# Performance work log

Measured on AMD Instinct MI355X. Metric: run time of the kernel, lower is better.

Reference implementation:

```python
import jax, jax.numpy as jnp
import numpy as np

NODES_PER_GRAPH = 116
HEADS = 2
D_HEAD = 116  # out_channels per head
HID = 256
B = 512
N = B * NODES_PER_GRAPH
DEG = 8
E = N * DEG
D_OUT = HEADS * D_HEAD  # 232


def setup_inputs() -> dict:
    key = jax.random.key(0)
    ks = jax.random.split(key, 6)
    h_flat = jax.random.normal(ks[0], (N, HID), dtype=jnp.float32)
    # every node receives DEG edges from random nodes within its own 116-node graph
    dst = jnp.repeat(jnp.arange(N, dtype=jnp.int64), DEG)
    offs = jax.random.randint(ks[1], (E,), 0, NODES_PER_GRAPH, dtype=jnp.int64)
    src = (dst // NODES_PER_GRAPH) * NODES_PER_GRAPH + offs
    edge_index = jnp.stack([src, dst], axis=0)
    batch_index = jnp.repeat(jnp.arange(B, dtype=jnp.int64), NODES_PER_GRAPH)
    s = 1.0 / np.sqrt(HID)
    Wq = jax.random.normal(ks[2], (HID, D_OUT), dtype=jnp.float32) * s
    Wk = jax.random.normal(ks[3], (HID, D_OUT), dtype=jnp.float32) * s
    Wv = jax.random.normal(ks[4], (HID, D_OUT), dtype=jnp.float32) * s
    Ws = jax.random.normal(ks[5], (HID, D_OUT), dtype=jnp.float32) * s
    return {"h_flat": h_flat, "edge_index": edge_index, "batch_index": batch_index,
            "Wq": Wq, "Wk": Wk, "Wv": Wv, "Ws": Ws}


def _graph_transformer_layer(h, edge_index, Wq, Wk, Wv, Ws):
    # PyG TransformerConv-style multi-head edge attention, concat heads + root skip.
    n = h.shape[0]
    q = (h @ Wq).reshape(n, HEADS, D_HEAD)
    k = (h @ Wk).reshape(n, HEADS, D_HEAD)
    v = (h @ Wv).reshape(n, HEADS, D_HEAD)
    src, dst = edge_index[0], edge_index[1]
    # per-edge scores [E, H]
    scores = jnp.einsum('ehd,ehd->eh', q[dst], k[src]) / np.sqrt(D_HEAD)
    # segment softmax over incoming edges of each dst node
    m = jax.ops.segment_max(scores, dst, num_segments=n)
    m = jnp.where(jnp.isfinite(m), m, 0.0)
    ex = jnp.exp(scores - m[dst])
    denom = jax.ops.segment_sum(ex, dst, num_segments=n)
    alpha_e = ex / (denom[dst] + 1e-16)
    msg = alpha_e[:, :, None] * v[src]                      # [E, H, Dh]
    attn = jax.ops.segment_sum(msg, dst, num_segments=n)    # [N, H, Dh]
    return attn.reshape(n, D_OUT) + h @ Ws


def reference(h_flat, edge_index, batch_index, Wq, Wk, Wv, Ws):
    n = h_flat.shape[0]
    b = n // NODES_PER_GRAPH
    h_proj = _graph_transformer_layer(h_flat, edge_index, Wq, Wk, Wv, Ws)  # [N, 232]
    e = h_proj.mean(axis=-1)                                 # [N]
    # scatter_softmax over per-graph node segments
    em = jax.ops.segment_max(e, batch_index, num_segments=b)
    ee = jnp.exp(e - em[batch_index])
    es = jax.ops.segment_sum(ee, batch_index, num_segments=b)
    alpha = ee / es[batch_index]                             # [N]
    h_weighted = alpha[:, None] * h_proj                     # [N, 232]
    alpha_map = alpha.reshape(b, NODES_PER_GRAPH)            # [B, 116]
    return alpha_map, h_weighted
```

## Files before the change

### kernel.cpp

```cpp
#include <hip/hip_runtime.h>

#define NODES  116
#define HEADS  2
#define DH     116
#define HID    256
#define NGRAPH 512
#define NN     (NGRAPH*NODES)
#define DEG    8
#define DOUT   (HEADS*DH)
#define RSTR   136

typedef short  s8v  __attribute__((ext_vector_type(8)));
typedef float  f4v  __attribute__((ext_vector_type(4)));

static __device__ __forceinline__ float bf2f(unsigned short u) {
    union { unsigned int i; float f; } c; c.i = ((unsigned int)u) << 16; return c.f;
}
static __device__ __forceinline__ unsigned short f2bf(float f) {
    union { float f; unsigned int u; } c; c.f = f;
    unsigned int u = c.u;
    unsigned int r = (u + 0x7FFFu + ((u >> 16) & 1u)) >> 16;
    return (unsigned short)r;
}

#define GLD_LDS16(gptr, lptr) \
    __builtin_amdgcn_global_load_lds((const __attribute__((address_space(1))) void*)(gptr), \
                                     (__attribute__((address_space(3))) void*)(lptr), 16, 0, 0)

__global__ __launch_bounds__(256) void prep_w(const float* __restrict__ Wq,
                                              const float* __restrict__ Wk,
                                              const float* __restrict__ Wv,
                                              const float* __restrict__ Ws,
                                              unsigned short* __restrict__ wt)
{
    unsigned int f = blockIdx.x * 256 + threadIdx.x;
    unsigned int n    = f & 127;
    unsigned int quad = (f >> 7) & 3;
    unsigned int kb   = (f >> 9) & 7;
    unsigned int ch   = (f >> 12) & 3;
    unsigned int hd   = f >> 14;
    unsigned short o[8] = {0,0,0,0,0,0,0,0};
    if (n < NODES) {
        unsigned int col = hd * DH + n;
        unsigned int k   = kb * 32 + quad * 8;
        const float* W = (ch == 0) ? Wq : (ch == 1) ? Wk : (ch == 2) ? Wv : Ws;
        #pragma unroll
        for (int i = 0; i < 8; i++)
            o[i] = f2bf(W[(size_t)(k + i) * DOUT + col]);
    }
    *(uint4*)(wt + (size_t)f * 8) = *(const uint4*)o;
}

__global__ __launch_bounds__(1024, 8) void k1_gemm(
    const float* __restrict__ h,
    const unsigned short* __restrict__ wt,
    unsigned short* __restrict__ qkvs)
{
    __shared__ __align__(16) unsigned short stA[8*4*116*8 + 96];
    __shared__ __align__(16) unsigned short stB[2*4096];

    const int b   = blockIdx.x;
    const int g   = b >> 1;
    const int hd  = b & 1;
    const int tid = threadIdx.x;
    const int w    = tid >> 6;
    const int lane = tid & 63;
    const int l15  = lane & 15;
    const int quad = lane >> 4;
    const int wm   = w >> 2;
    const int wn   = w & 3;

    {
        const int am = tid >> 3;
        const int q8 = tid & 7;
        if (am < NODES) {
            const float* hrow = h + ((size_t)g * NODES + am) * HID + q8 * 4;
            #pragma unroll
            for (int kb = 0; kb < 8; kb++) {
                float4 av = *(const float4*)(hrow + kb * 32);
                unsigned short o[4] = { f2bf(av.x), f2bf(av.y), f2bf(av.z), f2bf(av.w) };
                *(uint2*)(stA + kb * (4*116*8) + ((q8 >> 1) * 116 + am) * 8 + (q8 & 1) * 4) =
                    *(const uint2*)o;
            }
        }
    }

    const size_t wbase = (size_t)hd * 4 * 8 * 4096;

    if (w < 8) {
        const unsigned short* src = wt + wbase + w * 512;
        GLD_LDS16((const char*)src + lane * 16, (char*)stB + w * 1024);
    }
    __syncthreads();

    f4v acc[2][2];
    #pragma unroll
    for (int i = 0; i < 2; i++)
        #pragma unroll
        for (int j = 0; j < 2; j++)
            #pragma unroll
            for (int r = 0; r < 4; r++) acc[i][j][r] = 0.f;

    for (int t = 0; t < 32; t++) {
        const int kb = t & 7;
        const unsigned short* cur = stB + (t & 1) * 4096;
        if (t < 31 && w < 8) {
            const unsigned short* src = wt + wbase + (size_t)(t + 1) * 4096 + w * 512;
            GLD_LDS16((const char*)src + lane * 16,
                      (char*)stB + ((t & 1) ^ 1) * 8192 + w * 1024);
        }
        const unsigned short* sa = stA + kb * (4*116*8);
        s8v a0 = *(const s8v*)(sa + (quad * 116 + wm * 32 + l15) * 8);
        s8v a1 = *(const s8v*)(sa + (quad * 116 + wm * 32 + 16 + l15) * 8);
        s8v b0 = *(const s8v*)(cur + (quad * 128 + wn * 32 + l15) * 8);
        s8v b1 = *(const s8v*)(cur + (quad * 128 + wn * 32 + 16 + l15) * 8);
        acc[0][0] = __builtin_amdgcn_mfma_f32_16x16x32_bf16(a0, b0, acc[0][0], 0, 0, 0);
        acc[0][1] = __builtin_amdgcn_mfma_f32_16x16x32_bf16(a0, b1, acc[0][1], 0, 0, 0);
        acc[1][0] = __builtin_amdgcn_mfma_f32_16x16x32_bf16(a1, b0, acc[1][0], 0, 0, 0);
        acc[1][1] = __builtin_amdgcn_mfma_f32_16x16x32_bf16(a1, b1, acc[1][1], 0, 0, 0);
        if (kb == 7) {
            const int ch = t >> 3;
            #pragma unroll
            for (int i = 0; i < 2; i++) {
                #pragma unroll
                for (int j = 0; j < 2; j++) {
                    int col = wn * 32 + j * 16 + l15;
                    #pragma unroll
                    for (int r = 0; r < 4; r++) {
                        int row = wm * 32 + i * 16 + quad * 4 + r;
                        if (row < NODES && col < NODES)
                            qkvs[(((size_t)g * NODES + row) * 2 + hd) * 464 + ch * 116 + col] =
                                f2bf(acc[i][j][r]);
                        acc[i][j][r] = 0.f;
                    }
                }
            }
        }
        __syncthreads();
    }
}

__global__ __launch_bounds__(1024, 8) void k2_attn(
    const unsigned short* __restrict__ qkvs,
    const int* __restrict__ eidx,
    unsigned short* __restrict__ hpj,
    float* __restrict__ psums)
{
    __shared__ __align__(16) unsigned short ql[128*RSTR];
    __shared__ __align__(16) unsigned short kl[128*RSTR];
    __shared__ int   srcl[NODES*DEG];
    __shared__ float scf[NODES*DEG];

    const int b   = blockIdx.x;
    const int g   = b >> 1;
    const int hd  = b & 1;
    const int tid = threadIdx.x;
    const int w    = tid >> 6;
    const int lane = tid & 63;
    const int l15  = lane & 15;
    const int quad = lane >> 4;
    const int wm   = w >> 2;
    const int wn   = w & 3;

    if (tid < NODES * DEG)
        srcl[tid] = eidx[(size_t)g * NODES * DEG + tid] - g * NODES;

    const size_t nb = ((size_t)g * NODES) * 2 + hd;

    for (int f = tid; f < NODES * 29; f += 1024) {
        int r = f / 29, c = f - r * 29;
        *(uint2*)(ql + r * RSTR + c * 4) =
            *(const uint2*)(qkvs + (nb + (size_t)r * 2) * 464 + 0 * 116 + c * 4);
        *(uint2*)(kl + r * RSTR + c * 4) =
            *(const uint2*)(qkvs + (nb + (size_t)r * 2) * 464 + 1 * 116 + c * 4);
    }
    for (int f = tid; f < 128 * 3; f += 1024) {
        int r = f / 3, j = f - r * 3;
        *(uint2*)(ql + r * RSTR + 116 + j * 4) = make_uint2(0u, 0u);
        *(uint2*)(kl + r * RSTR + 116 + j * 4) = make_uint2(0u, 0u);
    }
    __syncthreads();

    f4v sacc[2][2];
    #pragma unroll
    for (int i = 0; i < 2; i++)
        #pragma unroll
        for (int j = 0; j < 2; j++)
            #pragma unroll
            for (int r = 0; r < 4; r++) sacc[i][j][r] = 0.f;
    #pragma unroll
    for (int ks = 0; ks < 4; ks++) {
        s8v a0 = *(const s8v*)(ql + (wm * 32 + l15) * RSTR + ks * 32 + quad * 8);
        s8v a1 = *(const s8v*)(ql + (wm * 32 + 16 + l15) * RSTR + ks * 32 + quad * 8);
        s8v b0 = *(const s8v*)(kl + (wn * 32 + l15) * RSTR + ks * 32 + quad * 8);
        s8v b1 = *(const s8v*)(kl + (wn * 32 + 16 + l15) * RSTR + ks * 32 + quad * 8);
        sacc[0][0] = __builtin_amdgcn_mfma_f32_16x16x32_bf16(a0, b0, sacc[0][0], 0, 0, 0);
        sacc[0][1] = __builtin_amdgcn_mfma_f32_16x16x32_bf16(a0, b1, sacc[0][1], 0, 0, 0);
        sacc[1][0] = __builtin_amdgcn_mfma_f32_16x16x32_bf16(a1, b0, sacc[1][0], 0, 0, 0);
        sacc[1][1] = __builtin_amdgcn_mfma_f32_16x16x32_bf16(a1, b1, sacc[1][1], 0, 0, 0);
    }
    #pragma unroll
    for (int i = 0; i < 2; i++) {
        #pragma unroll
        for (int r = 0; r < 4; r++) {
            int row = wm * 32 + i * 16 + quad * 4 + r;
            if (row < NODES) {
                #pragma unroll
                for (int j = 0; j < 2; j++) {
                    int col = wn * 32 + j * 16 + l15;
                    #pragma unroll
                    for (int e = 0; e < DEG; e++)
                        if (srcl[row * DEG + e] == col)
                            scf[row * DEG + e] = sacc[i][j][r];
                }
            }
        }
    }
    __syncthreads();

    for (int f = tid; f < 128 * RSTR / 8; f += 1024)
        *(uint4*)(kl + (size_t)f * 8) = make_uint4(0u, 0u, 0u, 0u);
    for (int f = tid; f < NODES * 29; f += 1024) {
        int r = f / 29, c = f - r * 29;
        uint2 vv = *(const uint2*)(qkvs + (nb + (size_t)r * 2) * 464 + 2 * 116 + c * 4);
        const unsigned short* vp = (const unsigned short*)&vv;
        #pragma unroll
        for (int i = 0; i < 4; i++)
            ql[(c * 4 + i) * RSTR + r] = vp[i];
    }
    if (tid < 12 * 17) {
        int r = 116 + tid / 17, c = tid - (tid / 17) * 17;
        *(uint4*)(ql + r * RSTR + c * 8) = make_uint4(0u, 0u, 0u, 0u);
    }
    __syncthreads();

    if (tid < NODES * DEG) {
        float s = scf[tid] * 0.09284766908852594f;
        float m = s;
        m = fmaxf(m, __shfl_xor(m, 1));
        m = fmaxf(m, __shfl_xor(m, 2));
        m = fmaxf(m, __shfl_xor(m, 4));
        float e = __expf(s - m);
        float sum = e;
        sum += __shfl_xor(sum, 1);
        sum += __shfl_xor(sum, 2);
        sum += __shfl_xor(sum, 4);
        scf[tid] = e / sum;
    }
    __syncthreads();

    if (tid < NODES) {
        #pragma unroll
        for (int j = 0; j < DEG; j++) {
            int sj = srcl[tid * DEG + j];
            bool first = true;
            for (int jj = 0; jj < j; jj++) first = first && (srcl[tid * DEG + jj] != sj);
            if (first) {
                float a = scf[tid * DEG + j];
                for (int jj = j + 1; jj < DEG; jj++)
                    if (srcl[tid * DEG + jj] == sj) a += scf[tid * DEG + jj];
                kl[tid * RSTR + sj] = f2bf(a);
            }
        }
    }
    __syncthreads();

    f4v accs[2][2];
    #pragma unroll
    for (int i = 0; i < 2; i++)
        #pragma unroll
        for (int j = 0; j < 2; j++)
            #pragma unroll
            for (int r = 0; r < 4; r++) accs[i][j][r] = 0.f;
    #pragma unroll
    for (int ks = 0; ks < 4; ks++) {
        s8v a0 = *(const s8v*)(kl + (wm * 32 + l15) * RSTR + ks * 32 + quad * 8);
        s8v a1 = *(const s8v*)(kl + (wm * 32 + 16 + l15) * RSTR + ks * 32 + quad * 8);
        s8v b0 = *(const s8v*)(ql + (wn * 32 + l15) * RSTR + ks * 32 + quad * 8);
        s8v b1 = *(const s8v*)(ql + (wn * 32 + 16 + l15) * RSTR + ks * 32 + quad * 8);
        accs[0][0] = __builtin_amdgcn_mfma_f32_16x16x32_bf16(a0, b0, accs[0][0], 0, 0, 0);
        accs[0][1] = __builtin_amdgcn_mfma_f32_16x16x32_bf16(a0, b1, accs[0][1], 0, 0, 0);
        accs[1][0] = __builtin_amdgcn_mfma_f32_16x16x32_bf16(a1, b0, accs[1][0], 0, 0, 0);
        accs[1][1] = __builtin_amdgcn_mfma_f32_16x16x32_bf16(a1, b1, accs[1][1], 0, 0, 0);
    }
    __syncthreads();

    for (int f = tid; f < NODES * 29; f += 1024) {
        int r = f / 29, c = f - r * 29;
        *(uint2*)(kl + r * RSTR + c * 4) =
            *(const uint2*)(qkvs + (nb + (size_t)r * 2) * 464 + 3 * 116 + c * 4);
    }
    __syncthreads();

    #pragma unroll
    for (int i = 0; i < 2; i++) {
        #pragma unroll
        for (int j = 0; j < 2; j++) {
            int col = wn * 32 + j * 16 + l15;
            #pragma unroll
            for (int r = 0; r < 4; r++) {
                int row = wm * 32 + i * 16 + quad * 4 + r;
                float v = accs[i][j][r];
                if (row < NODES && col < NODES) v += bf2f(kl[row * RSTR + col]);
                ql[row * RSTR + col] = f2bf(v);
            }
        }
    }
    __syncthreads();

    if (tid < NODES * DEG) {
        const int i   = tid >> 3;
        const int seg = tid & 7;
        float rs = 0.0f;
        #pragma unroll
        for (int t = 0; t < 2; t++) {
            int gi = seg + t * 8;
            if (gi < 15) {
                const s8v v8 = *(const s8v*)(ql + i * RSTR + gi * 8);
                #pragma unroll
                for (int e = 0; e < 8; e++) rs += bf2f((unsigned short)v8[e]);
            }
        }
        rs += __shfl_xor(rs, 1);
        rs += __shfl_xor(rs, 2);
        rs += __shfl_xor(rs, 4);
        if (seg == 0) psums[((size_t)hd * NGRAPH + g) * NODES + i] = rs;
    }
    for (int f = tid; f < NODES * 29; f += 1024) {
        int r  = f / 29;
        int gi = f - r * 29;
        *(uint2*)(hpj + ((size_t)(g * NODES + r)) * DOUT + hd * DH + gi * 4) =
            *(const uint2*)(ql + r * RSTR + gi * 4);
    }
}

__global__ __launch_bounds__(256) void pool_k3(const unsigned short* __restrict__ hp,
                                               const float* __restrict__ psums,
                                               float* __restrict__ out_alpha,
                                               float* __restrict__ out_hw)
{
    __shared__ float ew[NODES];
    __shared__ float alph[NODES];
    __shared__ float red[2];

    const int g   = blockIdx.x;
    const int tid = threadIdx.x;

    if (tid < NODES)
        ew[tid] = (psums[(size_t)g * NODES + tid] +
                   psums[((size_t)NGRAPH + g) * NODES + tid]) * (1.0f / DOUT);
    __syncthreads();
    if (tid < 64) {
        float a = ew[tid];
        float b = (tid + 64 < NODES) ? ew[tid + 64] : -1e30f;
        float mm = fmaxf(a, b);
        #pragma unroll
        for (int off = 32; off > 0; off >>= 1) mm = fmaxf(mm, __shfl_down(mm, off));
        if (tid == 0) red[0] = mm;
    }
    __syncthreads();
    if (tid < NODES) ew[tid] = __expf(ew[tid] - red[0]);
    __syncthreads();
    if (tid < 64) {
        float a = ew[tid] + ((tid + 64 < NODES) ? ew[tid + 64] : 0.0f);
        #pragma unroll
        for (int off = 32; off > 0; off >>= 1) a += __shfl_down(a, off);
        if (tid == 0) red[1] = a;
    }
    __syncthreads();
    if (tid < NODES) {
        float al = ew[tid] / red[1];
        alph[tid] = al;
        out_alpha[(size_t)g * NODES + tid] = al;
    }
    __syncthreads();

    for (int f = tid; f < NODES * 58; f += 256) {
        int r  = f / 58;
        int gi = f - r * 58;
        float al = alph[r];
        uint2 hv = *(const uint2*)(hp + ((size_t)(g * NODES + r)) * DOUT + gi * 4);
        float4 o = make_float4(al * bf2f((unsigned short)(hv.x & 0xFFFF)),
                               al * bf2f((unsigned short)(hv.x >> 16)),
                               al * bf2f((unsigned short)(hv.y & 0xFFFF)),
                               al * bf2f((unsigned short)(hv.y >> 16)));
        *(float4*)(out_hw + ((size_t)(g * NODES + r)) * DOUT + gi * 4) = o;
    }
}

__global__ __launch_bounds__(1024, 4) void fused_all(
    const float* __restrict__ h,
    const unsigned short* __restrict__ wt,
    const int* __restrict__ eidx,
    unsigned short* __restrict__ hp,
    float* __restrict__ out_alpha,
    float* __restrict__ out_hw)
{
    __shared__ __align__(16) unsigned short stA[8*4096];
    __shared__ __align__(16) unsigned short ovl[2*128*RSTR];
    __shared__ int   srcl[NODES*DEG];
    __shared__ float scf[NODES*DEG];
    __shared__ float ps[2][NODES];
    __shared__ float red[2];

    unsigned short* const ql = ovl;
    unsigned short* const kl = ovl + 128 * RSTR;

    const int g   = blockIdx.x;
    const int tid = threadIdx.x;
    const int w    = tid >> 6;
    const int lane = tid & 63;
    const int l15  = lane & 15;
    const int quad = lane >> 4;
    const int wm   = w >> 2;
    const int wn   = w & 3;

    if (tid < NODES * DEG)
        srcl[tid] = eidx[(size_t)g * NODES * DEG + tid] - g * NODES;

    {
        const int am = tid >> 3;
        const int q8 = tid & 7;
        long grow = (long)g * NODES + am;
        if (grow >= NN) grow = NN - 1;
        const float* hrow = h + (size_t)grow * HID + q8 * 4;
        const int aoff = ((q8 >> 1) * 128 + am) * 8 + (q8 & 1) * 4;
        float4 a8[8];
        #pragma unroll
        for (int kb = 0; kb < 8; kb++) a8[kb] = *(const float4*)(hrow + kb * 32);
        #pragma unroll
        for (int kb = 0; kb < 8; kb++) {
            unsigned short o[4] = { f2bf(a8[kb].x), f2bf(a8[kb].y),
                                    f2bf(a8[kb].z), f2bf(a8[kb].w) };
            *(uint2*)(stA + kb * 4096 + aoff) = *(const uint2*)o;
        }
    }

    #pragma unroll
    for (int hd = 0; hd < 2; hd++) {
        const size_t wbase = (size_t)hd * 4 * 8 * 4096;

        f4v accq[2][2], acck[2][2], accv[2][2], accs[2][2];
        #pragma unroll
        for (int i = 0; i < 2; i++)
            #pragma unroll
            for (int j = 0; j < 2; j++)
                #pragma unroll
                for (int r = 0; r < 4; r++) {
                    accq[i][j][r] = 0.f; acck[i][j][r] = 0.f;
                    accv[i][j][r] = 0.f; accs[i][j][r] = 0.f;
                }

        #pragma unroll
        for (int j = 0; j < 2; j++) {
            int c = w * 2 + j;
            int ch = c >> 3, sub = c & 7;
            const unsigned short* src = wt + wbase + ((size_t)(ch * 8)) * 4096 + sub * 512;
            GLD_LDS16((const char*)src + lane * 16, (char*)ovl + c * 1024);
        }
        __syncthreads();

        #pragma unroll
        for (int kb = 0; kb < 8; kb++) {
            const unsigned short* curb = ovl + (kb & 1) * 16384;
            unsigned short* nxtb = ovl + ((kb & 1) ^ 1) * 16384;
            if (kb < 7) {
                #pragma unroll
                for (int j = 0; j < 2; j++) {
                    int c = w * 2 + j;
                    int ch = c >> 3, sub = c & 7;
                    const unsigned short* src = wt + wbase + ((size_t)(ch * 8 + kb + 1)) * 4096 + sub * 512;
                    GLD_LDS16((const char*)src + lane * 16, (char*)nxtb + c * 1024);
                }
            }
            const unsigned short* sa = stA + kb * 4096;
            s8v a0 = *(const s8v*)(sa + (quad * 128 + wm * 32 + l15) * 8);
            s8v a1 = *(const s8v*)(sa + (quad * 128 + wm * 32 + 16 + l15) * 8);
            #define CHUNK_MFMA(ACC, CH) { \
                s8v b0 = *(const s8v*)(curb + (CH) * 4096 + (quad * 128 + wn * 32 + l15) * 8); \
                s8v b1 = *(const s8v*)(curb + (CH) * 4096 + (quad * 128 + wn * 32 + 16 + l15) * 8); \
                ACC[0][0] = __builtin_amdgcn_mfma_f32_16x16x32_bf16(a0, b0, ACC[0][0], 0, 0, 0); \
                ACC[0][1] = __builtin_amdgcn_mfma_f32_16x16x32_bf16(a0, b1, ACC[0][1], 0, 0, 0); \
                ACC[1][0] = __builtin_amdgcn_mfma_f32_16x16x32_bf16(a1, b0, ACC[1][0], 0, 0, 0); \
                ACC[1][1] = __builtin_amdgcn_mfma_f32_16x16x32_bf16(a1, b1, ACC[1][1], 0, 0, 0); }
            CHUNK_MFMA(accq, 0)
            CHUNK_MFMA(acck, 1)
            CHUNK_MFMA(accv, 2)
            CHUNK_MFMA(accs, 3)
            #undef CHUNK_MFMA
            __syncthreads();
        }

        #pragma unroll
        for (int i = 0; i < 2; i++) {
            #pragma unroll
            for (int j = 0; j < 2; j++) {
                int col = wn * 32 + j * 16 + l15;
                #pragma unroll
                for (int r = 0; r < 4; r++) {
                    int row = wm * 32 + i * 16 + quad * 4 + r;
                    ql[row * RSTR + col] = (col < NODES) ? f2bf(accq[i][j][r]) : 0;
                    kl[row * RSTR + col] = (col < NODES) ? f2bf(acck[i][j][r]) : 0;
                }
            }
        }
        __syncthreads();

        f4v sacc[2][2];
        #pragma unroll
        for (int i = 0; i < 2; i++)
            #pragma unroll
            for (int j = 0; j < 2; j++)
                #pragma unroll
                for (int r = 0; r < 4; r++) sacc[i][j][r] = 0.f;
        #pragma unroll
        for (int ks = 0; ks < 4; ks++) {
            s8v a0 = *(const s8v*)(ql + (wm * 32 + l15) * RSTR + ks * 32 + quad * 8);
            s8v a1 = *(const s8v*)(ql + (wm * 32 + 16 + l15) * RSTR + ks * 32 + quad * 8);
            s8v b0 = *(const s8v*)(kl + (wn * 32 + l15) * RSTR + ks * 32 + quad * 8);
            s8v b1 = *(const s8v*)(kl + (wn * 32 + 16 + l15) * RSTR + ks * 32 + quad * 8);
            sacc[0][0] = __builtin_amdgcn_mfma_f32_16x16x32_bf16(a0, b0, sacc[0][0], 0, 0, 0);
            sacc[0][1] = __builtin_amdgcn_mfma_f32_16x16x32_bf16(a0, b1, sacc[0][1], 0, 0, 0);
            sacc[1][0] = __builtin_amdgcn_mfma_f32_16x16x32_bf16(a1, b0, sacc[1][0], 0, 0, 0);
            sacc[1][1] = __builtin_amdgcn_mfma_f32_16x16x32_bf16(a1, b1, sacc[1][1], 0, 0, 0);
        }
        #pragma unroll
        for (int i = 0; i < 2; i++) {
            #pragma unroll
            for (int r = 0; r < 4; r++) {
                int row = wm * 32 + i * 16 + quad * 4 + r;
                if (row < NODES) {
                    #pragma unroll
                    for (int j = 0; j < 2; j++) {
                        int col = wn * 32 + j * 16 + l15;
                        #pragma unroll
                        for (int e = 0; e < DEG; e++)
                            if (srcl[row * DEG + e] == col)
                                scf[row * DEG + e] = sacc[i][j][r];
                    }
                }
            }
        }
        __syncthreads();

        for (int f = tid; f < 128 * RSTR / 8; f += 1024)
            *(uint4*)(kl + (size_t)f * 8) = make_uint4(0u, 0u, 0u, 0u);
        #pragma unroll
        for (int i = 0; i < 2; i++) {
            #pragma unroll
            for (int j = 0; j < 2; j++) {
                int col = wn * 32 + j * 16 + l15;
                #pragma unroll
                for (int r = 0; r < 4; r++) {
                    int row = wm * 32 + i * 16 + quad * 4 + r;
                    ql[col * RSTR + row] = (row < NODES) ? f2bf(accv[i][j][r]) : 0;
                }
            }
        }
        __syncthreads();

        if (tid < NODES * DEG) {
            float s = scf[tid] * 0.09284766908852594f;
            float m = s;
            m = fmaxf(m, __shfl_xor(m, 1));
            m = fmaxf(m, __shfl_xor(m, 2));
            m = fmaxf(m, __shfl_xor(m, 4));
            float e = __expf(s - m);
            float sum = e;
            sum += __shfl_xor(sum, 1);
            sum += __shfl_xor(sum, 2);
            sum += __shfl_xor(sum, 4);
            scf[tid] = e / sum;
        }
        __syncthreads();

        if (tid < NODES) {
            #pragma unroll
            for (int j = 0; j < DEG; j++) {
                int sj = srcl[tid * DEG + j];
                bool first = true;
                for (int jj = 0; jj < j; jj++) first = first && (srcl[tid * DEG + jj] != sj);
                if (first) {
                    float a = scf[tid * DEG + j];
                    for (int jj = j + 1; jj < DEG; jj++)
                        if (srcl[tid * DEG + jj] == sj) a += scf[tid * DEG + jj];
                    kl[tid * RSTR + sj] = f2bf(a);
                }
            }
        }
        __syncthreads();

        #pragma unroll
        for (int ks = 0; ks < 4; ks++) {
            s8v a0 = *(const s8v*)(kl + (wm * 32 + l15) * RSTR + ks * 32 + quad * 8);
            s8v a1 = *(const s8v*)(kl + (wm * 32 + 16 + l15) * RSTR + ks * 32 + quad * 8);
            s8v b0 = *(const s8v*)(ql + (wn * 32 + l15) * RSTR + ks * 32 + quad * 8);
            s8v b1 = *(const s8v*)(ql + (wn * 32 + 16 + l15) * RSTR + ks * 32 + quad * 8);
            accs[0][0] = __builtin_amdgcn_mfma_f32_16x16x32_bf16(a0, b0, accs[0][0], 0, 0, 0);
            accs[0][1] = __builtin_amdgcn_mfma_f32_16x16x32_bf16(a0, b1, accs[0][1], 0, 0, 0);
            accs[1][0] = __builtin_amdgcn_mfma_f32_16x16x32_bf16(a1, b0, accs[1][0], 0, 0, 0);
            accs[1][1] = __builtin_amdgcn_mfma_f32_16x16x32_bf16(a1, b1, accs[1][1], 0, 0, 0);
        }
        __syncthreads();

        #pragma unroll
        for (int i = 0; i < 2; i++) {
            #pragma unroll
            for (int j = 0; j < 2; j++) {
                int col = wn * 32 + j * 16 + l15;
                #pragma unroll
                for (int r = 0; r < 4; r++) {
                    int row = wm * 32 + i * 16 + quad * 4 + r;
                    ql[row * RSTR + col] = f2bf(accs[i][j][r]);
                }
            }
        }
        __syncthreads();

        if (tid < NODES * DEG) {
            const int i   = tid >> 3;
            const int seg = tid & 7;
            float rs = 0.0f;
            #pragma unroll
            for (int t = 0; t < 2; t++) {
                int gi = seg + t * 8;
                if (gi < 15) {
                    const s8v v8 = *(const s8v*)(ql + i * RSTR + gi * 8);
                    #pragma unroll
                    for (int e = 0; e < 8; e++) rs += bf2f((unsigned short)v8[e]);
                }
            }
            rs += __shfl_xor(rs, 1);
            rs += __shfl_xor(rs, 2);
            rs += __shfl_xor(rs, 4);
            if (seg == 0) ps[hd][i] = rs;
        }
        if (hd == 0) {
            for (int f = tid; f < NODES * 29; f += 1024) {
                int r  = f / 29;
                int gi = f - r * 29;
                *(uint2*)(hp + ((size_t)g * NODES + r) * 116 + gi * 4) =
                    *(const uint2*)(ql + r * RSTR + gi * 4);
            }
        }
        __syncthreads();
    }

    if (tid < NODES) scf[tid] = (ps[0][tid] + ps[1][tid]) * (1.0f / DOUT);
    __syncthreads();
    if (tid < 64) {
        float a = scf[tid];
        float b = (tid + 64 < NODES) ? scf[tid + 64] : -1e30f;
        float mm = fmaxf(a, b);
        #pragma unroll
        for (int off = 32; off > 0; off >>= 1) mm = fmaxf(mm, __shfl_down(mm, off));
        if (tid == 0) red[0] = mm;
    }
    __syncthreads();
    if (tid < NODES) scf[tid] = __expf(scf[tid] - red[0]);
    __syncthreads();
    if (tid < 64) {
        float a = scf[tid] + ((tid + 64 < NODES) ? scf[tid + 64] : 0.0f);
        #pragma unroll
        for (int off = 32; off > 0; off >>= 1) a += __shfl_down(a, off);
        if (tid == 0) red[1] = a;
    }
    __syncthreads();
    if (tid < NODES) {
        float al = scf[tid] / red[1];
        scf[tid] = al;
        out_alpha[(size_t)g * NODES + tid] = al;
    }
    __syncthreads();
    for (int f = tid; f < NODES * 58; f += 1024) {
        int r  = f / 58;
        int gi = f - r * 58;
        float al = scf[r];
        float4 o;
        if (gi < 29) {
            uint2 hv = *(const uint2*)(hp + ((size_t)g * NODES + r) * 116 + gi * 4);
            o = make_float4(al * bf2f((unsigned short)(hv.x & 0xFFFF)),
                            al * bf2f((unsigned short)(hv.x >> 16)),
                            al * bf2f((unsigned short)(hv.y & 0xFFFF)),
                            al * bf2f((unsigned short)(hv.y >> 16)));
        } else {
            const unsigned short* hv = ql + r * RSTR + (gi - 29) * 4;
            o = make_float4(al * bf2f(hv[0]), al * bf2f(hv[1]),
                            al * bf2f(hv[2]), al * bf2f(hv[3]));
        }
        *(float4*)(out_hw + ((size_t)g * NODES + r) * DOUT + gi * 4) = o;
    }
}

extern "C" void kernel_launch(void* const* d_in, const int* in_sizes, int n_in,
                              void* d_out, int out_size, void* d_ws, size_t ws_size,
                              hipStream_t stream)
{
    const float* h    = (const float*)d_in[0];
    const int*   eidx = (const int*)d_in[1];
    const float* Wq   = (const float*)d_in[3];
    const float* Wk   = (const float*)d_in[4];
    const float* Wv   = (const float*)d_in[5];
    const float* Ws   = (const float*)d_in[6];

    float* out_alpha = (float*)d_out;
    float* out_hw    = out_alpha + NN;

    const size_t WT_ELS   = 262144;
    const size_t QKVS_ELS = (size_t)NN * 2 * 464;
    const size_t HPJ_ELS  = (size_t)NN * DOUT;
    const size_t NEED = (WT_ELS + QKVS_ELS + HPJ_ELS) * 2 + (size_t)2 * NGRAPH * NODES * 4;

    unsigned short* wt = (unsigned short*)d_ws;
    prep_w<<<128, 256, 0, stream>>>(Wq, Wk, Wv, Ws, wt);

    if (ws_size >= NEED) {
        unsigned short* qkvs = wt + WT_ELS;
        unsigned short* hpj  = qkvs + QKVS_ELS;
        float*          ps   = (float*)(hpj + HPJ_ELS);
        k1_gemm<<<2*NGRAPH, 1024, 0, stream>>>(h, wt, qkvs);
        k2_attn<<<2*NGRAPH, 1024, 0, stream>>>(qkvs, eidx, hpj, ps);
        pool_k3<<<NGRAPH, 256, 0, stream>>>(hpj, ps, out_alpha, out_hw);
    } else {
        unsigned short* hp = wt + WT_ELS;
        fused_all<<<NGRAPH, 1024, 0, stream>>>(h, wt, eidx, hp, out_alpha, out_hw);
    }
}
```

Baseline: 251.8 us.

## Fuse QKVS projection GEMM into attention kernel, pre-convert h to bf16

Merges the projection GEMM and the attention kernel into one 512-thread kernel per (graph, head). Each Q/K/V/S chunk is computed directly into shared-memory tiles, which removes the global qkvs intermediate round-trip. A separate prep kernel converts h to bf16 once, and the fused kernel reads A and B operands straight from global memory rather than staging them through LDS. Trade-offs: h is re-read for each of the four chunks, there are more registers per thread and fewer threads per block, and an extra launch is added.

```diff
diff --git a/kernel.cpp b/kernel.cpp
--- a/kernel.cpp
+++ b/kernel.cpp
@@ -51,13 +51,28 @@
     *(uint4*)(wt + (size_t)f * 8) = *(const uint4*)o;
 }
 
-__global__ __launch_bounds__(1024, 8) void k1_gemm(
-    const float* __restrict__ h,
+__global__ __launch_bounds__(256) void prep_hb(const float* __restrict__ h,
+                                               unsigned short* __restrict__ hb)
+{
+    size_t i = ((size_t)blockIdx.x * 256 + threadIdx.x) * 8;
+    float4 a = *(const float4*)(h + i);
+    float4 b = *(const float4*)(h + i + 4);
+    unsigned short o[8] = { f2bf(a.x), f2bf(a.y), f2bf(a.z), f2bf(a.w),
+                            f2bf(b.x), f2bf(b.y), f2bf(b.z), f2bf(b.w) };
+    *(uint4*)(hb + i) = *(const uint4*)o;
+}
+
+__global__ __launch_bounds__(512, 4) void k_fused(
+    const unsigned short* __restrict__ hb,
     const unsigned short* __restrict__ wt,
-    unsigned short* __restrict__ qkvs)
+    const int* __restrict__ eidx,
+    unsigned short* __restrict__ hpj,
+    float* __restrict__ psums)
 {
-    __shared__ __align__(16) unsigned short stA[8*4*116*8 + 96];
-    __shared__ __align__(16) unsigned short stB[2*4096];
+    __shared__ __align__(16) unsigned short ql[128*RSTR];
+    __shared__ __align__(16) unsigned short kl[128*RSTR];
+    __shared__ __align__(16) short srcl[NODES*DEG];
+    __shared__ float scf[NODES*DEG];
 
     const int b   = blockIdx.x;
     const int g   = b >> 1;
@@ -67,137 +82,87 @@
     const int lane = tid & 63;
     const int l15  = lane & 15;
     const int quad = lane >> 4;
-    const int wm   = w >> 2;
-    const int wn   = w & 3;
-
-    {
-        const int am = tid >> 3;
-        const int q8 = tid & 7;
-        if (am < NODES) {
-            const float* hrow = h + ((size_t)g * NODES + am) * HID + q8 * 4;
-            #pragma unroll
-            for (int kb = 0; kb < 8; kb++) {
-                float4 av = *(const float4*)(hrow + kb * 32);
-                unsigned short o[4] = { f2bf(av.x), f2bf(av.y), f2bf(av.z), f2bf(av.w) };
-                *(uint2*)(stA + kb * (4*116*8) + ((q8 >> 1) * 116 + am) * 8 + (q8 & 1) * 4) =
-                    *(const uint2*)o;
-            }
-        }
-    }
-
-    const size_t wbase = (size_t)hd * 4 * 8 * 4096;
-
-    if (w < 8) {
-        const unsigned short* src = wt + wbase + w * 512;
-        GLD_LDS16((const char*)src + lane * 16, (char*)stB + w * 1024);
-    }
-    __syncthreads();
-
-    f4v acc[2][2];
+    const int wm   = w >> 1;
+    const int wn   = w & 1;
+
+    #pragma unroll
+    for (int p = 0; p < 2; p++) {
+        int f = tid + p * 512;
+        if (f < NODES * DEG)
+            srcl[f] = (short)(eidx[(size_t)g * NODES * DEG + f] - g * NODES);
+    }
+
+    long gr0 = (long)g * NODES + wm * 32 + l15;      if (gr0 >= NN) gr0 = NN - 1;
+    long gr1 = (long)g * NODES + wm * 32 + 16 + l15; if (gr1 >= NN) gr1 = NN - 1;
+    const unsigned short* ha0 = hb + (size_t)gr0 * HID;
+    const unsigned short* ha1 = hb + (size_t)gr1 * HID;
+    const unsigned short* wchb = wt + (size_t)hd * 4 * 8 * 4096
+                                    + (quad * 128 + wn * 64 + l15) * 8;
+
+    #define GEMM_CHUNK(CH, ACC) { \
+        _Pragma("unroll") \
+        for (int i_ = 0; i_ < 2; i_++) \
+            _Pragma("unroll") \
+            for (int j_ = 0; j_ < 4; j_++) \
+                _Pragma("unroll") \
+                for (int r_ = 0; r_ < 4; r_++) ACC[i_][j_][r_] = 0.f; \
+        _Pragma("unroll") \
+        for (int kb = 0; kb < 8; kb++) { \
+            s8v a0 = *(const s8v*)(ha0 + kb * 32 + quad * 8); \
+            s8v a1 = *(const s8v*)(ha1 + kb * 32 + quad * 8); \
+            _Pragma("unroll") \
+            for (int j = 0; j < 4; j++) { \
+                s8v bj = *(const s8v*)(wchb + ((CH) * 8 + kb) * 4096 + j * 128); \
+                ACC[0][j] = __builtin_amdgcn_mfma_f32_16x16x32_bf16(a0, bj, ACC[0][j], 0, 0, 0); \
+                ACC[1][j] = __builtin_amdgcn_mfma_f32_16x16x32_bf16(a1, bj, ACC[1][j], 0, 0, 0); \
+            } \
+        } }
+
+    f4v acc[2][4];
+
+    GEMM_CHUNK(0, acc)
     #pragma unroll
     for (int i = 0; i < 2; i++)
         #pragma unroll
-        for (int j = 0; j < 2; j++)
-            #pragma unroll
-            for (int r = 0; r < 4; r++) acc[i][j][r] = 0.f;
-
-    for (int t = 0; t < 32; t++) {
-        const int kb = t & 7;
-        const unsigned short* cur = stB + (t & 1) * 4096;
-        if (t < 31 && w < 8) {
-            const unsigned short* src = wt + wbase + (size_t)(t + 1) * 4096 + w * 512;
-            GLD_LDS16((const char*)src + lane * 16,
-                      (char*)stB + ((t & 1) ^ 1) * 8192 + w * 1024);
-        }
-        const unsigned short* sa = stA + kb * (4*116*8);
-        s8v a0 = *(const s8v*)(sa + (quad * 116 + wm * 32 + l15) * 8);
-        s8v a1 = *(const s8v*)(sa + (quad * 116 + wm * 32 + 16 + l15) * 8);
-        s8v b0 = *(const s8v*)(cur + (quad * 128 + wn * 32 + l15) * 8);
-        s8v b1 = *(const s8v*)(cur + (quad * 128 + wn * 32 + 16 + l15) * 8);
-        acc[0][0] = __builtin_amdgcn_mfma_f32_16x16x32_bf16(a0, b0, acc[0][0], 0, 0, 0);
-        acc[0][1] = __builtin_amdgcn_mfma_f32_16x16x32_bf16(a0, b1, acc[0][1], 0, 0, 0);
-        acc[1][0] = __builtin_amdgcn_mfma_f32_16x16x32_bf16(a1, b0, acc[1][0], 0, 0, 0);
-        acc[1][1] = __builtin_amdgcn_mfma_f32_16x16x32_bf16(a1, b1, acc[1][1], 0, 0, 0);
-        if (kb == 7) {
-            const int ch = t >> 3;
-            #pragma unroll
-            for (int i = 0; i < 2; i++) {
-                #pragma unroll
-                for (int j = 0; j < 2; j++) {
-                    int col = wn * 32 + j * 16 + l15;
-                    #pragma unroll
-                    for (int r = 0; r < 4; r++) {
-                        int row = wm * 32 + i * 16 + quad * 4 + r;
-                        if (row < NODES && col < NODES)
-                            qkvs[(((size_t)g * NODES + row) * 2 + hd) * 464 + ch * 116 + col] =
-                                f2bf(acc[i][j][r]);
-                        acc[i][j][r] = 0.f;
-                    }
-                }
-            }
-        }
-        __syncthreads();
-    }
-}
-
-__global__ __launch_bounds__(1024, 8) void k2_attn(
-    const unsigned short* __restrict__ qkvs,
-    const int* __restrict__ eidx,
-    unsigned short* __restrict__ hpj,
-    float* __restrict__ psums)
-{
-    __shared__ __align__(16) unsigned short ql[128*RSTR];
-    __shared__ __align__(16) unsigned short kl[128*RSTR];
-    __shared__ int   srcl[NODES*DEG];
-    __shared__ float scf[NODES*DEG];
-
-    const int b   = blockIdx.x;
-    const int g   = b >> 1;
-    const int hd  = b & 1;
-    const int tid = threadIdx.x;
-    const int w    = tid >> 6;
-    const int lane = tid & 63;
-    const int l15  = lane & 15;
-    const int quad = lane >> 4;
-    const int wm   = w >> 2;
-    const int wn   = w & 3;
-
-    if (tid < NODES * DEG)
-        srcl[tid] = eidx[(size_t)g * NODES * DEG + tid] - g * NODES;
-
-    const size_t nb = ((size_t)g * NODES) * 2 + hd;
-
-    for (int f = tid; f < NODES * 29; f += 1024) {
-        int r = f / 29, c = f - r * 29;
-        *(uint2*)(ql + r * RSTR + c * 4) =
-            *(const uint2*)(qkvs + (nb + (size_t)r * 2) * 464 + 0 * 116 + c * 4);
-        *(uint2*)(kl + r * RSTR + c * 4) =
-            *(const uint2*)(qkvs + (nb + (size_t)r * 2) * 464 + 1 * 116 + c * 4);
-    }
-    for (int f = tid; f < 128 * 3; f += 1024) {
-        int r = f / 3, j = f - r * 3;
-        *(uint2*)(ql + r * RSTR + 116 + j * 4) = make_uint2(0u, 0u);
-        *(uint2*)(kl + r * RSTR + 116 + j * 4) = make_uint2(0u, 0u);
-    }
-    __syncthreads();
-
-    f4v sacc[2][2];
+        for (int j = 0; j < 4; j++) {
+            int col = wn * 64 + j * 16 + l15;
+            #pragma unroll
+            for (int r = 0; r < 4; r++) {
+                int row = wm * 32 + i * 16 + quad * 4 + r;
+                ql[row * RSTR + col] = (col < NODES) ? f2bf(acc[i][j][r]) : 0;
+            }
+        }
+    GEMM_CHUNK(1, acc)
     #pragma unroll
     for (int i = 0; i < 2; i++)
         #pragma unroll
-        for (int j = 0; j < 2; j++)
+        for (int j = 0; j < 4; j++) {
+            int col = wn * 64 + j * 16 + l15;
+            #pragma unroll
+            for (int r = 0; r < 4; r++) {
+                int row = wm * 32 + i * 16 + quad * 4 + r;
+                kl[row * RSTR + col] = (col < NODES) ? f2bf(acc[i][j][r]) : 0;
+            }
+        }
+    __syncthreads();
+
+    f4v sacc[2][4];
+    #pragma unroll
+    for (int i = 0; i < 2; i++)
+        #pragma unroll
+        for (int j = 0; j < 4; j++)
             #pragma unroll
             for (int r = 0; r < 4; r++) sacc[i][j][r] = 0.f;
     #pragma unroll
     for (int ks = 0; ks < 4; ks++) {
         s8v a0 = *(const s8v*)(ql + (wm * 32 + l15) * RSTR + ks * 32 + quad * 8);
         s8v a1 = *(const s8v*)(ql + (wm * 32 + 16 + l15) * RSTR + ks * 32 + quad * 8);
-        s8v b0 = *(const s8v*)(kl + (wn * 32 + l15) * RSTR + ks * 32 + quad * 8);
-        s8v b1 = *(const s8v*)(kl + (wn * 32 + 16 + l15) * RSTR + ks * 32 + quad * 8);
-        sacc[0][0] = __builtin_amdgcn_mfma_f32_16x16x32_bf16(a0, b0, sacc[0][0], 0, 0, 0);
-        sacc[0][1] = __builtin_amdgcn_mfma_f32_16x16x32_bf16(a0, b1, sacc[0][1], 0, 0, 0);
-        sacc[1][0] = __builtin_amdgcn_mfma_f32_16x16x32_bf16(a1, b0, sacc[1][0], 0, 0, 0);
-        sacc[1][1] = __builtin_amdgcn_mfma_f32_16x16x32_bf16(a1, b1, sacc[1][1], 0, 0, 0);
+        #pragma unroll
+        for (int j = 0; j < 4; j++) {
+            s8v bj = *(const s8v*)(kl + (wn * 64 + j * 16 + l15) * RSTR + ks * 32 + quad * 8);
+            sacc[0][j] = __builtin_amdgcn_mfma_f32_16x16x32_bf16(a0, bj, sacc[0][j], 0, 0, 0);
+            sacc[1][j] = __builtin_amdgcn_mfma_f32_16x16x32_bf16(a1, bj, sacc[1][j], 0, 0, 0);
+        }
     }
     #pragma unroll
     for (int i = 0; i < 2; i++) {
@@ -205,12 +170,13 @@
         for (int r = 0; r < 4; r++) {
             int row = wm * 32 + i * 16 + quad * 4 + r;
             if (row < NODES) {
+                s8v sv = *(const s8v*)(srcl + row * DEG);
                 #pragma unroll
-                for (int j = 0; j < 2; j++) {
-                    int col = wn * 32 + j * 16 + l15;
+                for (int j = 0; j < 4; j++) {
+                    int col = wn * 64 + j * 16 + l15;
                     #pragma unroll
                     for (int e = 0; e < DEG; e++)
-                        if (srcl[row * DEG + e] == col)
+                        if ((int)sv[e] == col)
                             scf[row * DEG + e] = sacc[i][j][r];
                 }
             }
@@ -218,35 +184,25 @@
     }
     __syncthreads();
 
-    for (int f = tid; f < 128 * RSTR / 8; f += 1024)
+    #pragma unroll
+    for (int p = 0; p < 2; p++) {
+        int f = tid + p * 512;
+        if (f < NODES * DEG) {
+            float s = scf[f] * 0.09284766908852594f;
+            float m = s;
+            m = fmaxf(m, __shfl_xor(m, 1));
+            m = fmaxf(m, __shfl_xor(m, 2));
+            m = fmaxf(m, __shfl_xor(m, 4));
+            float e = __expf(s - m);
+            float sum = e;
+            sum += __shfl_xor(sum, 1);
+            sum += __shfl_xor(sum, 2);
+            sum += __shfl_xor(sum, 4);
+            scf[f] = e / sum;
+        }
+    }
+    for (int f = tid; f < 128 * RSTR / 8; f += 512)
         *(uint4*)(kl + (size_t)f * 8) = make_uint4(0u, 0u, 0u, 0u);
-    for (int f = tid; f < NODES * 29; f += 1024) {
-        int r = f / 29, c = f - r * 29;
-        uint2 vv = *(const uint2*)(qkvs + (nb + (size_t)r * 2) * 464 + 2 * 116 + c * 4);
-        const unsigned short* vp = (const unsigned short*)&vv;
-        #pragma unroll
-        for (int i = 0; i < 4; i++)
-            ql[(c * 4 + i) * RSTR + r] = vp[i];
-    }
-    if (tid < 12 * 17) {
-        int r = 116 + tid / 17, c = tid - (tid / 17) * 17;
-        *(uint4*)(ql + r * RSTR + c * 8) = make_uint4(0u, 0u, 0u, 0u);
-    }
-    __syncthreads();
-
-    if (tid < NODES * DEG) {
-        float s = scf[tid] * 0.09284766908852594f;
-        float m = s;
-        m = fmaxf(m, __shfl_xor(m, 1));
-        m = fmaxf(m, __shfl_xor(m, 2));
-        m = fmaxf(m, __shfl_xor(m, 4));
-        float e = __expf(s - m);
-        float sum = e;
-        sum += __shfl_xor(sum, 1);
-        sum += __shfl_xor(sum, 2);
-        sum += __shfl_xor(sum, 4);
-        scf[tid] = e / sum;
-    }
     __syncthreads();
 
     if (tid < NODES) {
@@ -263,75 +219,83 @@
             }
         }
     }
-    __syncthreads();
-
-    f4v accs[2][2];
+    GEMM_CHUNK(2, acc)
     #pragma unroll
     for (int i = 0; i < 2; i++)
         #pragma unroll
-        for (int j = 0; j < 2; j++)
-            #pragma unroll
-            for (int r = 0; r < 4; r++) accs[i][j][r] = 0.f;
+        for (int j = 0; j < 4; j++) {
+            int col = wn * 64 + j * 16 + l15;
+            #pragma unroll
+            for (int r = 0; r < 4; r++) {
+                int row = wm * 32 + i * 16 + quad * 4 + r;
+                ql[col * RSTR + row] = (row < NODES) ? f2bf(acc[i][j][r]) : 0;
+            }
+        }
+    __syncthreads();
+
+    f4v accS[2][4];
+    GEMM_CHUNK(3, accS)
+    #pragma unroll
+    for (int i = 0; i < 2; i++)
+        #pragma unroll
+        for (int j = 0; j < 4; j++)
+            #pragma unroll
+            for (int r = 0; r < 4; r++) acc[i][j][r] = 0.f;
     #pragma unroll
     for (int ks = 0; ks < 4; ks++) {
         s8v a0 = *(const s8v*)(kl + (wm * 32 + l15) * RSTR + ks * 32 + quad * 8);
         s8v a1 = *(const s8v*)(kl + (wm * 32 + 16 + l15) * RSTR + ks * 32 + quad * 8);
-        s8v b0 = *(const s8v*)(ql + (wn * 32 + l15) * RSTR + ks * 32 + quad * 8);
-        s8v b1 = *(const s8v*)(ql + (wn * 32 + 16 + l15) * RSTR + ks * 32 + quad * 8);
-        accs[0][0] = __builtin_amdgcn_mfma_f32_16x16x32_bf16(a0, b0, accs[0][0], 0, 0, 0);
-        accs[0][1] = __builtin_amdgcn_mfma_f32_16x16x32_bf16(a0, b1, accs[0][1], 0, 0, 0);
-        accs[1][0] = __builtin_amdgcn_mfma_f32_16x16x32_bf16(a1, b0, accs[1][0], 0, 0, 0);
-        accs[1][1] = __builtin_amdgcn_mfma_f32_16x16x32_bf16(a1, b1, accs[1][1], 0, 0, 0);
-    }
-    __syncthreads();
-
-    for (int f = tid; f < NODES * 29; f += 1024) {
-        int r = f / 29, c = f - r * 29;
-        *(uint2*)(kl + r * RSTR + c * 4) =
-            *(const uint2*)(qkvs + (nb + (size_t)r * 2) * 464 + 3 * 116 + c * 4);
-    }
-    __syncthreads();
-
-    #pragma unroll
-    for (int i = 0; i < 2; i++) {
-        #pragma unroll
-        for (int j = 0; j < 2; j++) {
-            int col = wn * 32 + j * 16 + l15;
+        #pragma unroll
+        for (int j = 0; j < 4; j++) {
+            s8v bj = *(const s8v*)(ql + (wn * 64 + j * 16 + l15) * RSTR + ks * 32 + quad * 8);
+            acc[0][j] = __builtin_amdgcn_mfma_f32_16x16x32_bf16(a0, bj, acc[0][j], 0, 0, 0);
+            acc[1][j] = __builtin_amdgcn_mfma_f32_16x16x32_bf16(a1, bj, acc[1][j], 0, 0, 0);
+        }
+    }
+    __syncthreads();
+
+    #pragma unroll
+    for (int i = 0; i < 2; i++)
+        #pragma unroll
+        for (int j = 0; j < 4; j++) {
+            int col = wn * 64 + j * 16 + l15;
             #pragma unroll
             for (int r = 0; r < 4; r++) {
                 int row = wm * 32 + i * 16 + quad * 4 + r;
-                float v = accs[i][j][r];
-                if (row < NODES && col < NODES) v += bf2f(kl[row * RSTR + col]);
-                ql[row * RSTR + col] = f2bf(v);
-            }
-        }
-    }
-    __syncthreads();
-
-    if (tid < NODES * DEG) {
-        const int i   = tid >> 3;
-        const int seg = tid & 7;
-        float rs = 0.0f;
-        #pragma unroll
-        for (int t = 0; t < 2; t++) {
-            int gi = seg + t * 8;
-            if (gi < 15) {
-                const s8v v8 = *(const s8v*)(ql + i * RSTR + gi * 8);
-                #pragma unroll
-                for (int e = 0; e < 8; e++) rs += bf2f((unsigned short)v8[e]);
-            }
-        }
-        rs += __shfl_xor(rs, 1);
-        rs += __shfl_xor(rs, 2);
-        rs += __shfl_xor(rs, 4);
-        if (seg == 0) psums[((size_t)hd * NGRAPH + g) * NODES + i] = rs;
-    }
-    for (int f = tid; f < NODES * 29; f += 1024) {
+                ql[row * RSTR + col] = f2bf(acc[i][j][r] + accS[i][j][r]);
+            }
+        }
+    __syncthreads();
+
+    #pragma unroll
+    for (int p = 0; p < 2; p++) {
+        int f = tid + p * 512;
+        if (f < NODES * DEG) {
+            const int i   = f >> 3;
+            const int seg = f & 7;
+            float rs = 0.0f;
+            #pragma unroll
+            for (int t = 0; t < 2; t++) {
+                int gi = seg + t * 8;
+                if (gi < 15) {
+                    const s8v v8 = *(const s8v*)(ql + i * RSTR + gi * 8);
+                    #pragma unroll
+                    for (int e = 0; e < 8; e++) rs += bf2f((unsigned short)v8[e]);
+                }
+            }
+            rs += __shfl_xor(rs, 1);
+            rs += __shfl_xor(rs, 2);
+            rs += __shfl_xor(rs, 4);
+            if (seg == 0) psums[((size_t)hd * NGRAPH + g) * NODES + i] = rs;
+        }
+    }
+    for (int f = tid; f < NODES * 29; f += 512) {
         int r  = f / 29;
         int gi = f - r * 29;
         *(uint2*)(hpj + ((size_t)(g * NODES + r)) * DOUT + hd * DH + gi * 4) =
             *(const uint2*)(ql + r * RSTR + gi * 4);
     }
+    #undef GEMM_CHUNK
 }
 
 __global__ __launch_bounds__(256) void pool_k3(const unsigned short* __restrict__ hp,
@@ -706,20 +670,20 @@
     float* out_alpha = (float*)d_out;
     float* out_hw    = out_alpha + NN;
 
-    const size_t WT_ELS   = 262144;
-    const size_t QKVS_ELS = (size_t)NN * 2 * 464;
-    const size_t HPJ_ELS  = (size_t)NN * DOUT;
-    const size_t NEED = (WT_ELS + QKVS_ELS + HPJ_ELS) * 2 + (size_t)2 * NGRAPH * NODES * 4;
+    const size_t WT_ELS  = 262144;
+    const size_t HB_ELS  = (size_t)NN * HID;
+    const size_t HPJ_ELS = (size_t)NN * DOUT;
+    const size_t NEED = (WT_ELS + HB_ELS + HPJ_ELS) * 2 + (size_t)2 * NGRAPH * NODES * 4;
 
     unsigned short* wt = (unsigned short*)d_ws;
     prep_w<<<128, 256, 0, stream>>>(Wq, Wk, Wv, Ws, wt);
 
     if (ws_size >= NEED) {
-        unsigned short* qkvs = wt + WT_ELS;
-        unsigned short* hpj  = qkvs + QKVS_ELS;
-        float*          ps   = (float*)(hpj + HPJ_ELS);
-        k1_gemm<<<2*NGRAPH, 1024, 0, stream>>>(h, wt, qkvs);
-        k2_attn<<<2*NGRAPH, 1024, 0, stream>>>(qkvs, eidx, hpj, ps);
+        unsigned short* hb  = wt + WT_ELS;
+        unsigned short* hpj = hb + HB_ELS;
+        float*          ps  = (float*)(hpj + HPJ_ELS);
+        prep_hb<<<(unsigned)(HB_ELS / (256 * 8)), 256, 0, stream>>>(h, hb);
+        k_fused<<<2 * NGRAPH, 512, 0, stream>>>(hb, wt, eidx, hpj, ps);
         pool_k3<<<NGRAPH, 256, 0, stream>>>(hpj, ps, out_alpha, out_hw);
     } else {
         unsigned short* hp = wt + WT_ELS;
```

After: 237.5 us. 1.06x faster.
